# Performance work log

Measured on AMD Instinct MI355X. Metric: run time of the kernel, lower is better.

The kernel has to match this reference:

```python
import jax, jax.numpy as jnp
import numpy as np

N = 200000   # 10000 graphs x 20 nodes, stacked
E = 3200000  # avg degree 16
F_IN = 4
H = 32
BN_EPS = 1e-5


def setup_inputs() -> dict:
    key = jax.random.key(0)
    ks = jax.random.split(key, 16)
    s = 0.1
    return {
        "x": jax.random.normal(ks[0], (N, F_IN), jnp.float32),
        "edge_index": jax.random.randint(ks[1], (2, E), 0, N, jnp.int64),
        "edge_weight": jax.random.uniform(ks[2], (E,), jnp.float32),
        "gcn1_w": jax.random.normal(ks[3], (F_IN, H), jnp.float32) * s,
        "gcn1_b": jnp.zeros((H,), jnp.float32),
        "gcn2_w": jax.random.normal(ks[4], (H, H), jnp.float32) * s,
        "gcn2_b": jnp.zeros((H,), jnp.float32),
        "bn1_gamma": jnp.ones((H,), jnp.float32),
        "bn1_beta": jnp.zeros((H,), jnp.float32),
        "bn1_mean": jnp.zeros((H,), jnp.float32),
        "bn1_var": jnp.ones((H,), jnp.float32),
        "bn2_gamma": jnp.ones((H,), jnp.float32),
        "bn2_beta": jnp.zeros((H,), jnp.float32),
        "bn2_mean": jnp.zeros((H,), jnp.float32),
        "bn2_var": jnp.ones((H,), jnp.float32),
        "lstm1_wih": jax.random.normal(ks[5], (4 * H, 2 * H), jnp.float32) * s,
        "lstm1_whh": jax.random.normal(ks[6], (4 * H, H), jnp.float32) * s,
        "lstm1_bih": jax.random.normal(ks[7], (4 * H,), jnp.float32) * s,
        "lstm1_bhh": jax.random.normal(ks[8], (4 * H,), jnp.float32) * s,
        "lstm2_wih": jax.random.normal(ks[9], (4 * H, H), jnp.float32) * s,
        "lstm2_whh": jax.random.normal(ks[10], (4 * H, H), jnp.float32) * s,
        "lstm2_bih": jax.random.normal(ks[11], (4 * H,), jnp.float32) * s,
        "lstm2_bhh": jax.random.normal(ks[12], (4 * H,), jnp.float32) * s,
        "lin_w": jax.random.normal(ks[13], (1, 2 * H + F_IN), jnp.float32) * s,
        "lin_b": jnp.zeros((1,), jnp.float32),
    }


def _gcn_conv(x, src, dst, ew, W, b, n):
    # GCNConv: x @ W, add self-loops (weight 1), symmetric normalization, scatter-add at dst.
    xw = x @ W
    loop = jnp.arange(n)
    s = jnp.concatenate([src, loop])
    d = jnp.concatenate([dst, loop])
    w = jnp.concatenate([ew, jnp.ones((n,), ew.dtype)])
    deg = jax.ops.segment_sum(w, d, num_segments=n)
    dinv = jnp.where(deg > 0, jax.lax.rsqrt(deg), 0.0)
    norm = dinv[s] * w * dinv[d]  # [E+N]
    out = jax.ops.segment_sum(norm[:, None] * xw[s], d, num_segments=n)
    return out + b


def _bn_eval(x, gamma, beta, mean, var):
    return (x - mean) * jax.lax.rsqrt(var + BN_EPS) * gamma + beta


def _lstm_step(x, wih, bih, bhh):
    # single timestep, zero initial (h, c): recurrent W_hh term vanishes.
    gates = x @ wih.T + bih + bhh
    i, f, g, o = jnp.split(gates, 4, axis=1)  # torch gate order i,f,g,o
    c = jax.nn.sigmoid(i) * jnp.tanh(g)
    return jax.nn.sigmoid(o) * jnp.tanh(c)


def reference(x, edge_index, edge_weight, gcn1_w, gcn1_b, gcn2_w, gcn2_b,
              bn1_gamma, bn1_beta, bn1_mean, bn1_var,
              bn2_gamma, bn2_beta, bn2_mean, bn2_var,
              lstm1_wih, lstm1_whh, lstm1_bih, lstm1_bhh,
              lstm2_wih, lstm2_whh, lstm2_bih, lstm2_bhh,
              lin_w, lin_b):
    n = x.shape[0]
    src, dst = edge_index[0], edge_index[1]
    # MPNNLSTM (window=1, eval mode: dropout=identity, BN uses running stats)
    h1 = _bn_eval(jax.nn.relu(_gcn_conv(x, src, dst, edge_weight, gcn1_w, gcn1_b, n)),
                  bn1_gamma, bn1_beta, bn1_mean, bn1_var)
    h2 = _bn_eval(jax.nn.relu(_gcn_conv(h1, src, dst, edge_weight, gcn2_w, gcn2_b, n)),
                  bn2_gamma, bn2_beta, bn2_mean, bn2_var)
    skip = jnp.concatenate([h1, h2], axis=1)  # [N, 2H]
    H1 = _lstm_step(skip, lstm1_wih, lstm1_bih, lstm1_bhh)  # [N, H]
    H2 = _lstm_step(H1, lstm2_wih, lstm2_bih, lstm2_bhh)    # [N, H]
    h = jnp.concatenate([H1, H2, x], axis=1)  # [N, 2H + F_IN]
    # RecurrentGCN head: relu + linear -> [N, 1]
    return jax.nn.relu(h) @ lin_w.T + lin_b
```

## Files before the change

kernel.cpp:

```cpp
#include <hip/hip_runtime.h>
#include <hip/hip_fp16.h>
#include <math.h>

#define BN_EPS 1e-5f
#define HF 32
#define BS 256
#define KEDGE 4096
#define MAXNB 800
#define SCAP 5504
#define WQ14 16383.0f
#define WQ22 4194303.0f

typedef _Float16 half8 __attribute__((ext_vector_type(8)));
typedef float f32x4 __attribute__((ext_vector_type(4)));
typedef float f32x2 __attribute__((ext_vector_type(2)));

__device__ __forceinline__ float fsig(float x) {
    return __builtin_amdgcn_rcpf(1.0f + __expf(-x));
}
__device__ __forceinline__ float ftanh(float x) {
    return 1.0f - 2.0f * __builtin_amdgcn_rcpf(1.0f + __expf(2.0f * x));
}


__device__ __forceinline__ float e4m3_to_f32_sw(unsigned v) {
    unsigned s = v & 0x80u, E = (v >> 3) & 0xFu, m = v & 7u;
    float r = E ? ldexpf((float)(8 + m), (int)E - 10) : ldexpf((float)m, -9);
    return s ? -r : r;
}

__device__ __forceinline__ unsigned f32_to_e4m3_sw(float x) {
    float ax = fabsf(x);
    unsigned s = x < 0.0f ? 0x80u : 0u;
    if (!(ax > 0.0f)) return s;
    if (ax >= 448.0f) return s | 0x7Eu;
    int e;
    float m = frexpf(ax, &e);
    int E = e - 1 + 7;
    if (E >= 1) {
        int q = (int)(m * 16.0f + 0.5f);
        if (q == 16) { q = 8; E += 1; if (E > 15) return s | 0x7Eu; }
        return s | (unsigned)(E << 3) | (unsigned)(q - 8);
    }
    int q = (int)(ax * 512.0f + 0.5f);
    if (q > 7) return s | 0x08u;
    return s | (unsigned)q;
}

__device__ __forceinline__ void dec8(uint2 r, float* f) {
#if __has_builtin(__builtin_amdgcn_cvt_pk_f32_fp8)
    f32x2 p0 = __builtin_amdgcn_cvt_pk_f32_fp8((int)r.x, false);
    f32x2 p1 = __builtin_amdgcn_cvt_pk_f32_fp8((int)r.x, true);
    f32x2 p2 = __builtin_amdgcn_cvt_pk_f32_fp8((int)r.y, false);
    f32x2 p3 = __builtin_amdgcn_cvt_pk_f32_fp8((int)r.y, true);
    f[0] = p0[0]; f[1] = p0[1]; f[2] = p1[0]; f[3] = p1[1];
    f[4] = p2[0]; f[5] = p2[1]; f[6] = p3[0]; f[7] = p3[1];
#else
#pragma unroll
    for (int k = 0; k < 4; ++k) f[k] = e4m3_to_f32_sw((r.x >> (8 * k)) & 0xFFu);
#pragma unroll
    for (int k = 0; k < 4; ++k) f[4 + k] = e4m3_to_f32_sw((r.y >> (8 * k)) & 0xFFu);
#endif
}

__device__ __forceinline__ uint2 enc8(const float* o) {
#if __has_builtin(__builtin_amdgcn_cvt_pk_fp8_f32)
    int w0 = 0, w1 = 0;
    w0 = __builtin_amdgcn_cvt_pk_fp8_f32(o[0], o[1], w0, false);
    w0 = __builtin_amdgcn_cvt_pk_fp8_f32(o[2], o[3], w0, true);
    w1 = __builtin_amdgcn_cvt_pk_fp8_f32(o[4], o[5], w1, false);
    w1 = __builtin_amdgcn_cvt_pk_fp8_f32(o[6], o[7], w1, true);
    return make_uint2((unsigned)w0, (unsigned)w1);
#else
    unsigned a = 0, b = 0;
#pragma unroll
    for (int k = 0; k < 4; ++k) a |= f32_to_e4m3_sw(o[k]) << (8 * k);
#pragma unroll
    for (int k = 0; k < 4; ++k) b |= f32_to_e4m3_sw(o[4 + k]) << (8 * k);
    return make_uint2(a, b);
#endif
}

__device__ __forceinline__ void gather_seg8(
        const unsigned* __restrict__ r, int cnp,
        const unsigned char* __restrict__ rows, int lane, float* acc) {
    const float qs = 1.0f / WQ14;
    uint4 na, nb;
    if (8 <= cnp) { na = *(const uint4*)(r); nb = *(const uint4*)(r + 4); }
    int e = 0;
    for (; e + 8 <= cnp; e += 8) {
        uint4 ua = na, ub = nb;
        if (e + 16 <= cnp) { na = *(const uint4*)(r + e + 8); nb = *(const uint4*)(r + e + 12); }
        unsigned u[8] = {ua.x, ua.y, ua.z, ua.w, ub.x, ub.y, ub.z, ub.w};
        uint2 rw[8];
#pragma unroll
        for (int q = 0; q < 8; ++q)
            rw[q] = ((const uint2*)(rows + ((size_t)(u[q] >> 14) << 5)))[lane];
        float nm[8];
#pragma unroll
        for (int q = 0; q < 8; ++q)
            nm[q] = (float)(u[q] & 16383u) * qs;
#pragma unroll
        for (int q = 0; q < 8; ++q) {
            float f[8];
            dec8(rw[q], f);
#pragma unroll
            for (int k = 0; k < 8; ++k) acc[k] += nm[q] * f[k];
        }
    }
}


__global__ __launch_bounds__(1024) void k_binsort(
        const int* __restrict__ src, const int* __restrict__ dst,
        const float* __restrict__ ew, int E, int NB, int bcap,
        int* __restrict__ gcur, uint2* __restrict__ recs) {
    __shared__ int hist[MAXNB], curs[MAXNB];

    int tid = threadIdx.x;
    int base = blockIdx.x * KEDGE;
    int cnt = min(KEDGE, E - base);

    for (int i = tid; i < NB; i += 1024) hist[i] = 0;
    __syncthreads();

    uint2 rec[4];
    int eb = base + tid * 4;
    int rem = cnt - tid * 4;
    if (rem >= 4) {
        int4 s0 = *(const int4*)(src + eb);
        int4 d0 = *(const int4*)(dst + eb);
        float4 w0 = *(const float4*)(ew + eb);
        int ss[4] = {s0.x, s0.y, s0.z, s0.w};
        int dd[4] = {d0.x, d0.y, d0.z, d0.w};
        float ww[4] = {w0.x, w0.y, w0.z, w0.w};
#pragma unroll
        for (int k = 0; k < 4; ++k) {
            unsigned q = (unsigned)(ww[k] * WQ22 + 0.5f);
            if (q > 4194303u) q = 4194303u;
            int b = dd[k] >> 8;
            rec[k] = make_uint2(((unsigned)ss[k] << 8) | (unsigned)(dd[k] & 255),
                                ((unsigned)b << 22) | q);
        }
    } else {
#pragma unroll
        for (int k = 0; k < 4; ++k) {
            if (k < rem) {
                int s = src[eb + k];
                int d = dst[eb + k];
                float w = ew[eb + k];
                unsigned q = (unsigned)(w * WQ22 + 0.5f);
                if (q > 4194303u) q = 4194303u;
                int b = d >> 8;
                rec[k] = make_uint2(((unsigned)s << 8) | (unsigned)(d & 255),
                                    ((unsigned)b << 22) | q);
            }
        }
    }
#pragma unroll
    for (int k = 0; k < 4; ++k)
        if (k < rem) atomicAdd(&hist[rec[k].y >> 22], 1);
    __syncthreads();

    for (int b = tid; b < NB; b += 1024) {
        int len = hist[b];
        curs[b] = len ? atomicAdd(&gcur[b], len) : 0;
    }
    __syncthreads();

#pragma unroll
    for (int k = 0; k < 4; ++k) {
        if (k < rem) {
            uint2 u = rec[k];
            int b = u.y >> 22;
            int off = atomicAdd(&curs[b], 1);
            if (off < bcap) recs[(size_t)b * bcap + off] = u;
        }
    }
}


__global__ __launch_bounds__(1024) void k_sortb(
        const uint2* __restrict__ recs, const int* __restrict__ gcur,
        int bcap, int bcap4,
        const float* __restrict__ x, const float* __restrict__ W1,
        unsigned* __restrict__ recs4, int* __restrict__ pstart,
        int* __restrict__ pcnt, float* __restrict__ dinv,
        unsigned char* __restrict__ y18,
        const float* __restrict__ wih1, const float* __restrict__ bih1,
        const float* __restrict__ bhh1, const float* __restrict__ wih2,
        const float* __restrict__ bih2, const float* __restrict__ bhh2,
        const float* __restrict__ bn1g, const float* __restrict__ bn1b,
        const float* __restrict__ bn1m, const float* __restrict__ bn1v,
        const float* __restrict__ bn2g, const float* __restrict__ bn2b,
        const float* __restrict__ bn2m, const float* __restrict__ bn2v,
        __half* __restrict__ wp1, __half* __restrict__ wp2,
        float* __restrict__ bsum1, float* __restrict__ bsum2,
        float* __restrict__ bnp, int n) {
    __shared__ uint2 srec[SCAP];
    __shared__ int hist[BS], excl4[BS], curs[BS], wsm[BS];
    __shared__ float sdv[BS];
    __shared__ float sW1[128];

    int b = blockIdx.x, tid = threadIdx.x;
    int cnt = min(gcur[b], bcap);
    const uint2* r = recs + (size_t)b * bcap;
    const float dq = 1.0f / WQ22;

    if (b == 0) {
        const int tg[6] = {0, 16, 64, 80, 96, 112};
        for (int idx = tid; idx < 9600; idx += 1024) {
            if (idx < 6144) {
                int t = idx >> 10, rm = idx & 1023;
                int kc = rm >> 9, rm2 = rm & 511;
                int lane = rm2 >> 3, j = rm2 & 7;
                int g = tg[t] + (lane & 15);
                int k = kc * 32 + (lane >> 4) * 8 + j;
                wp1[idx] = __float2half(wih1[g * 64 + k]);
            } else if (idx < 9216) {
                int i2 = idx - 6144;
                int t = i2 >> 9, rm2 = i2 & 511;
                int lane = rm2 >> 3, j = rm2 & 7;
                int g = tg[t] + (lane & 15);
                int k = (lane >> 4) * 8 + j;
                wp2[i2] = __float2half(wih2[g * 32 + k]);
            } else if (idx < 9344) {
                int i = idx - 9216;
                bsum1[i] = bih1[i] + bhh1[i];
            } else if (idx < 9472) {
                int i = idx - 9344;
                bsum2[i] = bih2[i] + bhh2[i];
            } else {
                int f2 = idx - 9472;
                int f = f2 & 31;
                if (f2 < 32) {
                    bnp[f2] = bn1g[f] * rsqrtf(bn1v[f] + BN_EPS);
                } else if (f2 < 64) {
                    float sc = bn1g[f] * rsqrtf(bn1v[f] + BN_EPS);
                    bnp[f2] = bn1b[f] - bn1m[f] * sc;
                } else if (f2 < 96) {
                    bnp[f2] = bn2g[f] * rsqrtf(bn2v[f] + BN_EPS);
                } else {
                    float sc = bn2g[f] * rsqrtf(bn2v[f] + BN_EPS);
                    bnp[f2] = bn2b[f] - bn2m[f] * sc;
                }
            }
        }
    }

    if (tid < BS) { hist[tid] = 0; wsm[tid] = 0; }
    if (tid >= 256 && tid < 384) sW1[tid - 256] = W1[tid - 256];
    __syncthreads();

    for (int i = tid; i < cnt; i += 1024) {
        uint2 u = r[i];
        if (i < SCAP) srec[i] = u;
        int dl = u.x & 255;
        atomicAdd(&hist[dl], 1);
        atomicAdd(&wsm[dl], (int)(u.y & 4194303u));
    }
    __syncthreads();

    if (tid < BS) {
        int g = b * BS + tid;
        sdv[tid] = (g < n) ? rsqrtf(1.0f + (float)wsm[tid] * dq) : 0.0f;
    }
    if (tid < 64) {
        int run = 0;
        for (int c = 0; c < BS; c += 64) {
            int idx = c + tid;
            int v = (hist[idx] + 7) & ~7;
            int incl = v;
#pragma unroll
            for (int o = 1; o < 64; o <<= 1) {
                int up = __shfl_up(incl, o, 64);
                if (tid >= o) incl += up;
            }
            int e = run + incl - v;
            excl4[idx] = e; curs[idx] = e;
            run += __shfl(incl, 63, 64);
        }
    }
    __syncthreads();

    unsigned* out4 = recs4 + (size_t)b * bcap4;
    for (int i = tid; i < cnt; i += 1024) {
        uint2 u = (i < SCAP) ? srec[i] : r[i];
        int dl = u.x & 255;
        int pos = atomicAdd(&curs[dl], 1);
        float qn = (float)(u.y & 4194303u) * dq * sdv[dl];
        unsigned q = (unsigned)(qn * WQ14 + 0.5f);
        if (q > 16383u) q = 16383u;
        out4[pos] = ((u.x >> 8) << 14) | q;
    }

    {
        int node = tid >> 2, q = tid & 3;
        int g = b * BS + node;
        if (g < n) {
            float4 xv = *(const float4*)(x + (size_t)g * 4);
            float sc = sdv[node];
            int f0 = q * 8;
            float o[8];
#pragma unroll
            for (int k = 0; k < 8; ++k)
                o[k] = sc * (xv.x * sW1[f0 + k] + xv.y * sW1[32 + f0 + k] +
                             xv.z * sW1[64 + f0 + k] + xv.w * sW1[96 + f0 + k]);
            ((uint2*)(y18 + ((size_t)g << 5)))[q] = enc8(o);
        }
    }

    if (tid < BS) {
        int g = b * BS + tid;
        int cnp = (hist[tid] + 7) & ~7;
        int end = excl4[tid] + hist[tid];
        int pend = excl4[tid] + cnp;
        for (int p2 = end; p2 < pend; ++p2) out4[p2] = 0u;
        if (g < n) {
            pstart[g] = b * bcap4 + excl4[tid];
            pcnt[g] = cnp;
            dinv[g] = sdv[tid];
        }
    }
}


__global__ __launch_bounds__(256) void k_g1w2(
        const unsigned* __restrict__ recs4, const int* __restrict__ pstart,
        const int* __restrict__ pcnt, const float* __restrict__ dinv,
        const unsigned char* __restrict__ y18, const float* __restrict__ W2,
        const float* __restrict__ bias, const float* __restrict__ bnsc,
        const float* __restrict__ bnsh,
        __half* __restrict__ skiph, unsigned char* __restrict__ A8, int n) {
    __shared__ float sW2[1024];
    __shared__ float sh1[64][33];
    int tid = threadIdx.x;

    int nl = tid >> 2;
    int g = blockIdx.x * 64 + nl;
    int lane = tid & 3;
    int fq = lane * 8;
    bool act = g < n;

    float dig = 0.0f;
    int cn = 0;
    const unsigned* r = recs4;
    uint2 sr = make_uint2(0u, 0u);
    if (act) {
        dig = dinv[g];
        cn = pcnt[g];
        r = recs4 + pstart[g];
        sr = ((const uint2*)(y18 + ((size_t)g << 5)))[lane];
    }

    for (int i = tid; i < 1024; i += 256) sW2[i] = W2[i];

    float acc[8];
#pragma unroll
    for (int k = 0; k < 8; ++k) acc[k] = 0.0f;

    if (act) {
        {
            float f[8];
            dec8(sr, f);
#pragma unroll
            for (int k = 0; k < 8; ++k) acc[k] = dig * f[k];
        }
        gather_seg8(r, cn, y18, lane, acc);
    }

    float o[8];
#pragma unroll
    for (int k = 0; k < 8; ++k) {
        float v = fmaxf(acc[k] + bias[fq + k], 0.0f);
        o[k] = v * bnsc[fq + k] + bnsh[fq + k];
        sh1[nl][fq + k] = o[k];
    }
    if (act) {
        union { __half h[8]; uint4 q; } hv;
#pragma unroll
        for (int k = 0; k < 8; ++k) hv.h[k] = __float2half(o[k]);
        *(uint4*)(skiph + (size_t)g * 32 + fq) = hv.q;
    }
    __syncthreads();

    if (act) {
        float a2[8];
#pragma unroll
        for (int j = 0; j < 8; ++j) a2[j] = 0.0f;
#pragma unroll 4
        for (int k = 0; k < 32; ++k) {
            float h = sh1[nl][k];
            const float* wr = sW2 + k * 32 + fq;
#pragma unroll
            for (int j = 0; j < 8; ++j) a2[j] += h * wr[j];
        }
#pragma unroll
        for (int j = 0; j < 8; ++j) a2[j] *= dig;
        ((uint2*)(A8 + ((size_t)g << 5)))[lane] = enc8(a2);
    }
}


__global__ __launch_bounds__(256) void k_g2head(
        const unsigned* __restrict__ recs4, const int* __restrict__ pstart,
        const int* __restrict__ pcnt, const float* __restrict__ dinv,
        const unsigned char* __restrict__ A8,
        const float* __restrict__ bias, const float* __restrict__ bnsc,
        const float* __restrict__ bnsh,
        const __half* __restrict__ skiph, const float* __restrict__ x,
        const __half* __restrict__ wp1, const __half* __restrict__ wp2,
        const float* __restrict__ bsum1, const float* __restrict__ bsum2,
        const float* __restrict__ lw, const float* __restrict__ lb,
        float* __restrict__ out, int n) {
    __shared__ __align__(16) __half h2s[64][40];
    __shared__ __align__(16) __half H1lds[4 * 16 * 40];
    int tid = threadIdx.x;
    int nl = tid >> 2;
    int g = blockIdx.x * 64 + nl;
    int lane = tid & 3;
    int fq = lane * 8;
    bool act = g < n;

    int w = tid >> 6, l = tid & 63;
    int quad = l >> 4, c = l & 15;
    int node_base = blockIdx.x * 64 + w * 16;
    int arow = node_base + c; if (arow > n - 1) arow = n - 1;
    int lr = arow - blockIdx.x * 64;
    half8 a0 = *(const half8*)(skiph + (size_t)arow * 32 + quad * 8);

    float dig = 0.0f;
    int cn = 0;
    const unsigned* r = recs4;
    uint2 sr = make_uint2(0u, 0u);
    if (act) {
        dig = dinv[g];
        cn = pcnt[g];
        r = recs4 + pstart[g];
        sr = ((const uint2*)(A8 + ((size_t)g << 5)))[lane];
    }

    float acc[8];
#pragma unroll
    for (int k = 0; k < 8; ++k) acc[k] = 0.0f;

    if (act) {
        {
            float f[8];
            dec8(sr, f);
#pragma unroll
            for (int k = 0; k < 8; ++k) acc[k] = dig * f[k];
        }
        gather_seg8(r, cn, A8, lane, acc);

        union { __half h[8]; uint4 q; } hv;
#pragma unroll
        for (int k = 0; k < 8; ++k) {
            float v = fmaxf(acc[k] + bias[fq + k], 0.0f);
            hv.h[k] = __float2half(v * bnsc[fq + k] + bnsh[fq + k]);
        }
        *(uint4*)(&h2s[nl][fq]) = hv.q;
    }
    __syncthreads();

    half8 a1 = *(const half8*)(&h2s[lr][quad * 8]);

    const half8* b1 = (const half8*)wp1;
    f32x4 d[6];
#pragma unroll
    for (int t = 0; t < 6; ++t) {
        f32x4 ac = {0.0f, 0.0f, 0.0f, 0.0f};
        ac = __builtin_amdgcn_mfma_f32_16x16x32_f16(a0, b1[(t * 2 + 0) * 64 + l], ac, 0, 0, 0);
        ac = __builtin_amdgcn_mfma_f32_16x16x32_f16(a1, b1[(t * 2 + 1) * 64 + l], ac, 0, 0, 0);
        d[t] = ac;
    }

    float bi0 = bsum1[c],      bi1 = bsum1[16 + c];
    float bg0 = bsum1[64 + c], bg1 = bsum1[80 + c];
    float bo0 = bsum1[96 + c], bo1 = bsum1[112 + c];
    float lwc0 = lw[c], lwc1 = lw[c + 16];

    float pa[4];
#pragma unroll
    for (int r2 = 0; r2 < 4; ++r2) {
        float cc0 = fsig(d[0][r2] + bi0) * ftanh(d[2][r2] + bg0);
        float h0 = fsig(d[4][r2] + bo0) * ftanh(cc0);
        float cc1 = fsig(d[1][r2] + bi1) * ftanh(d[3][r2] + bg1);
        float h1 = fsig(d[5][r2] + bo1) * ftanh(cc1);
        pa[r2] = fmaxf(h0, 0.0f) * lwc0 + fmaxf(h1, 0.0f) * lwc1;
        __half* hp = H1lds + (w * 16 + quad * 4 + r2) * 40;
        hp[c] = __float2half(h0);
        hp[c + 16] = __float2half(h1);
    }
    __syncthreads();

    half8 a2 = *(const half8*)(H1lds + (w * 16 + c) * 40 + quad * 8);

    const half8* b2 = (const half8*)wp2;
    f32x4 e2[6];
#pragma unroll
    for (int t = 0; t < 6; ++t) {
        f32x4 ac = {0.0f, 0.0f, 0.0f, 0.0f};
        e2[t] = __builtin_amdgcn_mfma_f32_16x16x32_f16(a2, b2[t * 64 + l], ac, 0, 0, 0);
    }

    float ci0 = bsum2[c],      ci1 = bsum2[16 + c];
    float cg0 = bsum2[64 + c], cg1 = bsum2[80 + c];
    float co0 = bsum2[96 + c], co1 = bsum2[112 + c];
    float lw2c0 = lw[32 + c], lw2c1 = lw[48 + c];
#pragma unroll
    for (int r2 = 0; r2 < 4; ++r2) {
        float cc0 = fsig(e2[0][r2] + ci0) * ftanh(e2[2][r2] + cg0);
        float h0 = fsig(e2[4][r2] + co0) * ftanh(cc0);
        float cc1 = fsig(e2[1][r2] + ci1) * ftanh(e2[3][r2] + cg1);
        float h1 = fsig(e2[5][r2] + co1) * ftanh(cc1);
        pa[r2] += fmaxf(h0, 0.0f) * lw2c0 + fmaxf(h1, 0.0f) * lw2c1;
    }

#pragma unroll
    for (int m = 1; m < 16; m <<= 1) {
#pragma unroll
        for (int r2 = 0; r2 < 4; ++r2) pa[r2] += __shfl_xor(pa[r2], m, 64);
    }

    if (c < 4) {
        int node = node_base + quad * 4 + c;
        if (node < n) {
            const float4 xv = *(const float4*)(x + (size_t)node * 4);
            out[node] = pa[c] + lb[0]
                + fmaxf(xv.x, 0.0f) * lw[64] + fmaxf(xv.y, 0.0f) * lw[65]
                + fmaxf(xv.z, 0.0f) * lw[66] + fmaxf(xv.w, 0.0f) * lw[67];
        }
    }
}


__global__ void k_initdeg(float* __restrict__ deg, int n) {
    int i = blockIdx.x * blockDim.x + threadIdx.x;
    if (i < n) deg[i] = 1.0f;
}

__global__ void k_deg_only(const int* __restrict__ dst, const float* __restrict__ ew,
                           float* __restrict__ deg, int E) {
    int e = blockIdx.x * blockDim.x + threadIdx.x;
    if (e < E) atomicAdd(&deg[dst[e]], ew[e]);
}

__global__ void k_dinv_f(float* __restrict__ deg, int n) {
    int i = blockIdx.x * blockDim.x + threadIdx.x;
    if (i < n) {
        float d = deg[i];
        deg[i] = d > 0.0f ? rsqrtf(d) : 0.0f;
    }
}

__global__ void k_xw1_f(const float* __restrict__ x, const float* __restrict__ W,
                        float* __restrict__ out, int n) {
    int idx = blockIdx.x * blockDim.x + threadIdx.x;
    if (idx >= n * HF) return;
    int nn = idx >> 5, f = idx & 31;
    const float4 xr = *(const float4*)(x + (size_t)nn * 4);
    out[idx] = xr.x * W[f] + xr.y * W[32 + f] + xr.z * W[64 + f] + xr.w * W[96 + f];
}

__global__ void k_xw2_f(const float* __restrict__ Hin, const float* __restrict__ W,
                        float* __restrict__ out, int n) {
    __shared__ float sW[32 * 32];
    __shared__ float sH[8][32];
    int tid = threadIdx.x;
    for (int i = tid; i < 1024; i += 256) sW[i] = W[i];
    int r = tid >> 5, f = tid & 31;
    int nn = blockIdx.x * 8 + r;
    if (nn < n) sH[r][f] = Hin[(size_t)nn * HF + f];
    __syncthreads();
    if (nn >= n) return;
    float acc = 0.0f;
#pragma unroll
    for (int k = 0; k < 32; ++k) acc += sH[r][k] * sW[k * 32 + f];
    out[(size_t)nn * HF + f] = acc;
}

__global__ void k_selfloop(const float* __restrict__ A, const float* __restrict__ dinv,
                           float* __restrict__ B, int n) {
    int idx = blockIdx.x * blockDim.x + threadIdx.x;
    if (idx >= n * HF) return;
    int nn = idx >> 5;
    float di = dinv[nn];
    B[idx] = di * di * A[idx];
}

__global__ void k_scatter(const int* __restrict__ src, const int* __restrict__ dst,
                          const float* __restrict__ ew, const float* __restrict__ dinv,
                          const float* __restrict__ A, float* __restrict__ B, int total) {
    int idx = blockIdx.x * blockDim.x + threadIdx.x;
    if (idx >= total) return;
    int e = idx >> 5, f = idx & 31;
    int s = src[e], d = dst[e];
    float norm = dinv[s] * ew[e] * dinv[d];
    atomicAdd(&B[d * HF + f], norm * A[s * HF + f]);
}

__global__ void k_post(const float* __restrict__ B, const float* __restrict__ bias,
                       const float* __restrict__ gamma, const float* __restrict__ beta,
                       const float* __restrict__ mean, const float* __restrict__ var,
                       float* __restrict__ Hout, int n) {
    int idx = blockIdx.x * blockDim.x + threadIdx.x;
    if (idx >= n * HF) return;
    int f = idx & 31;
    float v = fmaxf(B[idx] + bias[f], 0.0f);
    float sc = gamma[f] * rsqrtf(var[f] + BN_EPS);
    Hout[idx] = (v - mean[f]) * sc + beta[f];
}

__global__ __launch_bounds__(256) void k_head(
        const float* __restrict__ h1, const float* __restrict__ h2,
        const float* __restrict__ x,
        const float* __restrict__ wih1, const float* __restrict__ bih1, const float* __restrict__ bhh1,
        const float* __restrict__ wih2, const float* __restrict__ bih2, const float* __restrict__ bhh2,
        const float* __restrict__ lw, const float* __restrict__ lb,
        float* __restrict__ out, int n) {
    __shared__ float sH1[32 * 256];
    int tid = threadIdx.x;
    int nn = blockIdx.x * 256 + tid;
    if (nn >= n) return;

    const float4* a = (const float4*)(h1 + (size_t)nn * HF);
    const float4* b = (const float4*)(h2 + (size_t)nn * HF);
    float skip[64];
#pragma unroll
    for (int q = 0; q < 8; ++q) {
        float4 v = a[q];
        skip[4 * q] = v.x; skip[4 * q + 1] = v.y; skip[4 * q + 2] = v.z; skip[4 * q + 3] = v.w;
        float4 u = b[q];
        skip[32 + 4 * q] = u.x; skip[33 + 4 * q] = u.y; skip[34 + 4 * q] = u.z; skip[35 + 4 * q] = u.w;
    }

    float oa = lb[0];
#pragma unroll 1
    for (int j = 0; j < 32; ++j) {
        const float4* wi = (const float4*)(wih1 + (size_t)j * 64);
        const float4* wg = (const float4*)(wih1 + (size_t)(64 + j) * 64);
        const float4* wo = (const float4*)(wih1 + (size_t)(96 + j) * 64);
        float gi = bih1[j] + bhh1[j];
        float gg = bih1[64 + j] + bhh1[64 + j];
        float go = bih1[96 + j] + bhh1[96 + j];
#pragma unroll
        for (int q = 0; q < 16; ++q) {
            float4 aa = wi[q], bb = wg[q], cc4 = wo[q];
            float s0 = skip[4 * q], s1 = skip[4 * q + 1], s2 = skip[4 * q + 2], s3 = skip[4 * q + 3];
            gi += aa.x * s0 + aa.y * s1 + aa.z * s2 + aa.w * s3;
            gg += bb.x * s0 + bb.y * s1 + bb.z * s2 + bb.w * s3;
            go += cc4.x * s0 + cc4.y * s1 + cc4.z * s2 + cc4.w * s3;
        }
        float cc = fsig(gi) * ftanh(gg);
        float hh = fsig(go) * ftanh(cc);
        sH1[j * 256 + tid] = hh;
        oa += fmaxf(hh, 0.0f) * lw[j];
    }

#pragma unroll 1
    for (int j = 0; j < 32; ++j) {
        const float4* wi = (const float4*)(wih2 + (size_t)j * 32);
        const float4* wg = (const float4*)(wih2 + (size_t)(64 + j) * 32);
        const float4* wo = (const float4*)(wih2 + (size_t)(96 + j) * 32);
        float gi = bih2[j] + bhh2[j];
        float gg = bih2[64 + j] + bhh2[64 + j];
        float go = bih2[96 + j] + bhh2[96 + j];
#pragma unroll
        for (int q = 0; q < 8; ++q) {
            float4 aa = wi[q], bb = wg[q], cc4 = wo[q];
            float s0 = sH1[(4 * q) * 256 + tid], s1 = sH1[(4 * q + 1) * 256 + tid];
            float s2 = sH1[(4 * q + 2) * 256 + tid], s3 = sH1[(4 * q + 3) * 256 + tid];
            gi += aa.x * s0 + aa.y * s1 + aa.z * s2 + aa.w * s3;
            gg += bb.x * s0 + bb.y * s1 + bb.z * s2 + bb.w * s3;
            go += cc4.x * s0 + cc4.y * s1 + cc4.z * s2 + cc4.w * s3;
        }
        float cc = fsig(gi) * ftanh(gg);
        float hh = fsig(go) * ftanh(cc);
        oa += fmaxf(hh, 0.0f) * lw[32 + j];
    }

    const float4 xv = *(const float4*)(x + (size_t)nn * 4);
    oa += fmaxf(xv.x, 0.0f) * lw[64] + fmaxf(xv.y, 0.0f) * lw[65] +
          fmaxf(xv.z, 0.0f) * lw[66] + fmaxf(xv.w, 0.0f) * lw[67];
    out[nn] = oa;
}


extern "C" void kernel_launch(void* const* d_in, const int* in_sizes, int n_in,
                              void* d_out, int out_size, void* d_ws, size_t ws_size,
                              hipStream_t stream) {
    const float* x   = (const float*)d_in[0];
    const int*   ei  = (const int*)d_in[1];
    const float* ew  = (const float*)d_in[2];
    const float* g1w = (const float*)d_in[3];
    const float* g1b = (const float*)d_in[4];
    const float* g2w = (const float*)d_in[5];
    const float* g2b = (const float*)d_in[6];
    const float* bn1g = (const float*)d_in[7];
    const float* bn1b = (const float*)d_in[8];
    const float* bn1m = (const float*)d_in[9];
    const float* bn1v = (const float*)d_in[10];
    const float* bn2g = (const float*)d_in[11];
    const float* bn2b = (const float*)d_in[12];
    const float* bn2m = (const float*)d_in[13];
    const float* bn2v = (const float*)d_in[14];
    const float* w1ih = (const float*)d_in[15];
    const float* b1ih = (const float*)d_in[17];
    const float* b1hh = (const float*)d_in[18];
    const float* w2ih = (const float*)d_in[19];
    const float* b2ih = (const float*)d_in[21];
    const float* b2hh = (const float*)d_in[22];
    const float* lw   = (const float*)d_in[23];
    const float* lb   = (const float*)d_in[24];
    float* out = (float*)d_out;

    const int N = in_sizes[0] / 4;
    const int E = in_sizes[2];
    const int* src = ei;
    const int* dst = ei + E;

    const int T = 256;
    const int NB = (N + BS - 1) / BS;
    long long meanb = ((long long)BS * E) / (N > 0 ? N : 1);
    int bcap = (int)(meanb + meanb / 4 + 128);
    bcap = (bcap + 7) & ~7;
    int bcap4 = bcap + 7 * BS;

    char* p = (char*)d_ws;
    auto alloc = [&](size_t bytes) { char* q = p; p += (bytes + 255) & ~(size_t)255; return q; };
    int*      gcur   = (int*)alloc(sizeof(int) * NB);
    uint2*    recs   = (uint2*)alloc(sizeof(uint2) * (size_t)NB * bcap);
    unsigned* recs4  = (unsigned*)alloc(sizeof(unsigned) * (size_t)NB * bcap4);
    float*    dinv   = (float*)alloc(sizeof(float) * N);
    int*      pstart = (int*)alloc(sizeof(int) * N);
    int*      pcnt   = (int*)alloc(sizeof(int) * N);
    unsigned char* y18 = (unsigned char*)alloc((size_t)N * HF);
    unsigned char* A8  = (unsigned char*)alloc((size_t)N * HF);
    __half*   skiph  = (__half*)alloc(sizeof(__half) * (size_t)N * 32);
    __half*   wp1    = (__half*)alloc(sizeof(__half) * 6144);
    __half*   wp2    = (__half*)alloc(sizeof(__half) * 3072);
    float*    bsum1  = (float*)alloc(sizeof(float) * 128);
    float*    bsum2  = (float*)alloc(sizeof(float) * 128);
    float*    bnp    = (float*)alloc(sizeof(float) * 128);
    size_t need = (size_t)(p - (char*)d_ws);

    int bN  = (N + T - 1) / T;
    int bE  = (E + T - 1) / T;
    int bNF = (N * HF + T - 1) / T;
    int bN8 = (N + 7) / 8;
    int bG  = (N + 63) / 64;
    int bBin = (E + KEDGE - 1) / KEDGE;

    if (ws_size >= need && NB <= MAXNB && N <= (1 << 18) && bcap <= SCAP) {
        hipMemsetAsync(gcur, 0, sizeof(int) * NB, stream);
        k_binsort<<<bBin, 1024, 0, stream>>>(src, dst, ew, E, NB, bcap, gcur, recs);
        k_sortb<<<NB, 1024, 0, stream>>>(recs, gcur, bcap, bcap4, x, g1w,
                                         recs4, pstart, pcnt, dinv, y18,
                                         w1ih, b1ih, b1hh, w2ih, b2ih, b2hh,
                                         bn1g, bn1b, bn1m, bn1v,
                                         bn2g, bn2b, bn2m, bn2v,
                                         wp1, wp2, bsum1, bsum2, bnp, N);

        k_g1w2<<<bG, T, 0, stream>>>(recs4, pstart, pcnt, dinv, y18, g2w,
                                     g1b, bnp, bnp + 32, skiph, A8, N);
        k_g2head<<<bG, T, 0, stream>>>(recs4, pstart, pcnt, dinv, A8,
                                       g2b, bnp + 64, bnp + 96,
                                       skiph, x, wp1, wp2, bsum1, bsum2,
                                       lw, lb, out, N);
    } else {
        size_t Npad = ((size_t)N + 255) & ~(size_t)255;
        float* fdinv = (float*)d_ws;
        float* fA = fdinv + Npad;
        float* fB = fA + (size_t)N * HF;
        float* fC = fB + (size_t)N * HF;
        int bEF = (int)(((long long)E * HF + T - 1) / T);
        int bH = (N + 255) / 256;

        k_initdeg<<<bN, T, 0, stream>>>(fdinv, N);
        k_deg_only<<<bE, T, 0, stream>>>(dst, ew, fdinv, E);
        k_dinv_f<<<bN, T, 0, stream>>>(fdinv, N);

        k_xw1_f<<<bNF, T, 0, stream>>>(x, g1w, fA, N);
        k_selfloop<<<bNF, T, 0, stream>>>(fA, fdinv, fB, N);
        k_scatter<<<bEF, T, 0, stream>>>(src, dst, ew, fdinv, fA, fB, E * HF);
        k_post<<<bNF, T, 0, stream>>>(fB, g1b, bn1g, bn1b, bn1m, bn1v, fC, N);

        k_xw2_f<<<bN8, T, 0, stream>>>(fC, g2w, fA, N);
        k_selfloop<<<bNF, T, 0, stream>>>(fA, fdinv, fB, N);
        k_scatter<<<bEF, T, 0, stream>>>(src, dst, ew, fdinv, fA, fB, E * HF);
        k_post<<<bNF, T, 0, stream>>>(fB, g2b, bn2g, bn2b, bn2m, bn2v, fB, N);

        k_head<<<bH, T, 0, stream>>>(fC, fB, x, w1ih, b1ih, b1hh, w2ih, b2ih, b2hh,
                                     lw, lb, out, N);
    }
}
```

Before: 266.8 us.

## Sort nodes by in-degree within each bucket to balance gather workloads

```diff
diff --git a/kernel.cpp b/kernel.cpp
--- a/kernel.cpp
+++ b/kernel.cpp
@@ -186,6 +186,7 @@
         const float* __restrict__ x, const float* __restrict__ W1,
         unsigned* __restrict__ recs4, int* __restrict__ pstart,
         int* __restrict__ pcnt, float* __restrict__ dinv,
+        int* __restrict__ perm,
         unsigned char* __restrict__ y18,
         const float* __restrict__ wih1, const float* __restrict__ bih1,
         const float* __restrict__ bhh1, const float* __restrict__ wih2,
@@ -199,8 +200,10 @@
         float* __restrict__ bnp, int n) {
     __shared__ uint2 srec[SCAP];
     __shared__ int hist[BS], excl4[BS], curs[BS], wsm[BS];
+    __shared__ int sperm[BS], slen[BS], segst[BS];
     __shared__ float sdv[BS];
     __shared__ float sW1[128];
+    __shared__ int dh[66];
 
     int b = blockIdx.x, tid = threadIdx.x;
     int cnt = min(gcur[b], bcap);
@@ -249,6 +252,7 @@
     }
 
     if (tid < BS) { hist[tid] = 0; wsm[tid] = 0; }
+    if (tid < 66) dh[tid] = 0;
     if (tid >= 256 && tid < 384) sW1[tid - 256] = W1[tid - 256];
     __syncthreads();
 
@@ -264,23 +268,43 @@
     if (tid < BS) {
         int g = b * BS + tid;
         sdv[tid] = (g < n) ? rsqrtf(1.0f + (float)wsm[tid] * dq) : 0.0f;
-    }
+        int key = (g < n) ? min(hist[tid], 63) : 64;
+        atomicAdd(&dh[key + 1], 1);
+    }
+    __syncthreads();
+    if (tid == 0) {
+#pragma unroll 1
+        for (int k = 1; k < 66; ++k) dh[k] += dh[k - 1];
+    }
+    __syncthreads();
+    if (tid < BS) {
+        int g = b * BS + tid;
+        int key = (g < n) ? min(hist[tid], 63) : 64;
+        int pos = atomicAdd(&dh[key], 1);
+        sperm[pos] = tid;
+        slen[pos] = hist[tid];
+    }
+    __syncthreads();
+
     if (tid < 64) {
         int run = 0;
         for (int c = 0; c < BS; c += 64) {
             int idx = c + tid;
-            int v = (hist[idx] + 7) & ~7;
+            int v = (slen[idx] + 7) & ~7;
             int incl = v;
 #pragma unroll
             for (int o = 1; o < 64; o <<= 1) {
                 int up = __shfl_up(incl, o, 64);
                 if (tid >= o) incl += up;
             }
-            int e = run + incl - v;
-            excl4[idx] = e; curs[idx] = e;
+            excl4[idx] = run + incl - v;
             run += __shfl(incl, 63, 64);
         }
     }
+    __syncthreads();
+    if (tid < BS) segst[sperm[tid]] = excl4[tid];
+    __syncthreads();
+    if (tid < BS) curs[tid] = segst[tid];
     __syncthreads();
 
     unsigned* out4 = recs4 + (size_t)b * bcap4;
@@ -311,16 +335,17 @@
     }
 
     if (tid < BS) {
-        int g = b * BS + tid;
-        int cnp = (hist[tid] + 7) & ~7;
-        int end = excl4[tid] + hist[tid];
+        int local = sperm[tid];
+        int g = b * BS + local;
+        int slot = b * BS + tid;
+        int cnp = (slen[tid] + 7) & ~7;
+        int end = excl4[tid] + slen[tid];
         int pend = excl4[tid] + cnp;
         for (int p2 = end; p2 < pend; ++p2) out4[p2] = 0u;
-        if (g < n) {
-            pstart[g] = b * bcap4 + excl4[tid];
-            pcnt[g] = cnp;
-            dinv[g] = sdv[tid];
-        }
+        perm[slot] = g;
+        pstart[slot] = b * bcap4 + excl4[tid];
+        pcnt[slot] = cnp;
+        if (g < n) dinv[g] = sdv[local];
     }
 }
 
@@ -328,6 +353,7 @@
 __global__ __launch_bounds__(256) void k_g1w2(
         const unsigned* __restrict__ recs4, const int* __restrict__ pstart,
         const int* __restrict__ pcnt, const float* __restrict__ dinv,
+        const int* __restrict__ perm,
         const unsigned char* __restrict__ y18, const float* __restrict__ W2,
         const float* __restrict__ bias, const float* __restrict__ bnsc,
         const float* __restrict__ bnsh,
@@ -337,9 +363,11 @@
     int tid = threadIdx.x;
 
     int nl = tid >> 2;
-    int g = blockIdx.x * 64 + nl;
+    int slot = blockIdx.x * 64 + nl;
     int lane = tid & 3;
     int fq = lane * 8;
+
+    int g = perm[slot];
     bool act = g < n;
 
     float dig = 0.0f;
@@ -348,8 +376,8 @@
     uint2 sr = make_uint2(0u, 0u);
     if (act) {
         dig = dinv[g];
-        cn = pcnt[g];
-        r = recs4 + pstart[g];
+        cn = pcnt[slot];
+        r = recs4 + pstart[slot];
         sr = ((const uint2*)(y18 + ((size_t)g << 5)))[lane];
     }
 
@@ -405,6 +433,7 @@
 __global__ __launch_bounds__(256) void k_g2head(
         const unsigned* __restrict__ recs4, const int* __restrict__ pstart,
         const int* __restrict__ pcnt, const float* __restrict__ dinv,
+        const int* __restrict__ perm,
         const unsigned char* __restrict__ A8,
         const float* __restrict__ bias, const float* __restrict__ bnsc,
         const float* __restrict__ bnsh,
@@ -417,17 +446,20 @@
     __shared__ __align__(16) __half H1lds[4 * 16 * 40];
     int tid = threadIdx.x;
     int nl = tid >> 2;
-    int g = blockIdx.x * 64 + nl;
+    int slot = blockIdx.x * 64 + nl;
     int lane = tid & 3;
     int fq = lane * 8;
+
+    int g = perm[slot];
     bool act = g < n;
 
     int w = tid >> 6, l = tid & 63;
     int quad = l >> 4, c = l & 15;
-    int node_base = blockIdx.x * 64 + w * 16;
-    int arow = node_base + c; if (arow > n - 1) arow = n - 1;
-    int lr = arow - blockIdx.x * 64;
-    half8 a0 = *(const half8*)(skiph + (size_t)arow * 32 + quad * 8);
+    int slot_base = blockIdx.x * 64 + w * 16;
+    int hslot = slot_base + c;
+    int hg = perm[hslot]; if (hg > n - 1) hg = n - 1;
+    int lr = hslot - blockIdx.x * 64;
+    half8 a0 = *(const half8*)(skiph + (size_t)hg * 32 + quad * 8);
 
     float dig = 0.0f;
     int cn = 0;
@@ -435,8 +467,8 @@
     uint2 sr = make_uint2(0u, 0u);
     if (act) {
         dig = dinv[g];
-        cn = pcnt[g];
-        r = recs4 + pstart[g];
+        cn = pcnt[slot];
+        r = recs4 + pstart[slot];
         sr = ((const uint2*)(A8 + ((size_t)g << 5)))[lane];
     }
 
@@ -524,7 +556,8 @@
     }
 
     if (c < 4) {
-        int node = node_base + quad * 4 + c;
+        int oslot = slot_base + quad * 4 + c;
+        int node = perm[oslot];
         if (node < n) {
             const float4 xv = *(const float4*)(x + (size_t)node * 4);
             out[node] = pa[c] + lb[0]
@@ -733,8 +766,9 @@
     uint2*    recs   = (uint2*)alloc(sizeof(uint2) * (size_t)NB * bcap);
     unsigned* recs4  = (unsigned*)alloc(sizeof(unsigned) * (size_t)NB * bcap4);
     float*    dinv   = (float*)alloc(sizeof(float) * N);
-    int*      pstart = (int*)alloc(sizeof(int) * N);
-    int*      pcnt   = (int*)alloc(sizeof(int) * N);
+    int*      pstart = (int*)alloc(sizeof(int) * (size_t)NB * BS);
+    int*      pcnt   = (int*)alloc(sizeof(int) * (size_t)NB * BS);
+    int*      perm   = (int*)alloc(sizeof(int) * (size_t)NB * BS);
     unsigned char* y18 = (unsigned char*)alloc((size_t)N * HF);
     unsigned char* A8  = (unsigned char*)alloc((size_t)N * HF);
     __half*   skiph  = (__half*)alloc(sizeof(__half) * (size_t)N * 32);
@@ -749,25 +783,25 @@
     int bE  = (E + T - 1) / T;
     int bNF = (N * HF + T - 1) / T;
     int bN8 = (N + 7) / 8;
-    int bG  = (N + 63) / 64;
+    int bG4 = NB * 4;
     int bBin = (E + KEDGE - 1) / KEDGE;
 
     if (ws_size >= need && NB <= MAXNB && N <= (1 << 18) && bcap <= SCAP) {
         hipMemsetAsync(gcur, 0, sizeof(int) * NB, stream);
         k_binsort<<<bBin, 1024, 0, stream>>>(src, dst, ew, E, NB, bcap, gcur, recs);
         k_sortb<<<NB, 1024, 0, stream>>>(recs, gcur, bcap, bcap4, x, g1w,
-                                         recs4, pstart, pcnt, dinv, y18,
+                                         recs4, pstart, pcnt, dinv, perm, y18,
                                          w1ih, b1ih, b1hh, w2ih, b2ih, b2hh,
                                          bn1g, bn1b, bn1m, bn1v,
                                          bn2g, bn2b, bn2m, bn2v,
                                          wp1, wp2, bsum1, bsum2, bnp, N);
 
-        k_g1w2<<<bG, T, 0, stream>>>(recs4, pstart, pcnt, dinv, y18, g2w,
-                                     g1b, bnp, bnp + 32, skiph, A8, N);
-        k_g2head<<<bG, T, 0, stream>>>(recs4, pstart, pcnt, dinv, A8,
-                                       g2b, bnp + 64, bnp + 96,
-                                       skiph, x, wp1, wp2, bsum1, bsum2,
-                                       lw, lb, out, N);
+        k_g1w2<<<bG4, T, 0, stream>>>(recs4, pstart, pcnt, dinv, perm, y18, g2w,
+                                      g1b, bnp, bnp + 32, skiph, A8, N);
+        k_g2head<<<bG4, T, 0, stream>>>(recs4, pstart, pcnt, dinv, perm, A8,
+                                        g2b, bnp + 64, bnp + 96,
+                                        skiph, x, wp1, wp2, bsum1, bsum2,
+                                        lw, lb, out, N);
     } else {
         size_t Npad = ((size_t)N + 255) & ~(size_t)255;
         float* fdinv = (float*)d_ws;
```

Result: slower. 286.4 us (+7.3%).
